# Kernel optimization log

Measured on AMD Instinct MI355X. Metric: run time of the kernel, lower is better.

The kernel has to match this reference:

```python
import jax, jax.numpy as jnp
import numpy as np

HEAD, DIM, R = 8, 256, 3
RA = (2 * R + 1) ** 2  # 49


def conv2d(x, w, b=None, pad=0, groups=1):
    y = jax.lax.conv_general_dilated(x, w, (1, 1), [(pad, pad), (pad, pad)],
                                     dimension_numbers=('NCHW', 'OIHW', 'NCHW'),
                                     feature_group_count=groups)
    return y if b is None else y + b[None, :, None, None]


def grid_sample(img, grid, mode, padding='zeros'):
    # img [B,C,H,W]; grid [B,Hg,Wg,2] with (x,y) in [-1,1]; align_corners=False.
    B, C, H, W = img.shape
    Hg, Wg = grid.shape[1], grid.shape[2]
    gx = ((grid[..., 0] + 1.0) * W - 1.0) / 2.0
    gy = ((grid[..., 1] + 1.0) * H - 1.0) / 2.0
    if padding == 'border':
        gx = jnp.clip(gx, 0.0, W - 1.0)
        gy = jnp.clip(gy, 0.0, H - 1.0)
    gx = gx.reshape(B, -1)
    gy = gy.reshape(B, -1)

    def gather(iy, ix):
        iyc = jnp.clip(iy, 0, H - 1)
        ixc = jnp.clip(ix, 0, W - 1)
        return jax.vmap(lambda im, a, b: im[:, a, b])(img, iyc, ixc)  # [B,C,N]

    def mask(iy, ix):
        if padding == 'border':
            return jnp.ones(iy.shape, img.dtype)
        return ((ix >= 0) & (ix < W) & (iy >= 0) & (iy < H)).astype(img.dtype)

    if mode == 'nearest':
        ix = jnp.round(gx).astype(jnp.int32)
        iy = jnp.round(gy).astype(jnp.int32)
        out = gather(iy, ix) * mask(iy, ix)[:, None, :]
    else:  # bilinear
        x0f = jnp.floor(gx); y0f = jnp.floor(gy)
        wx = gx - x0f; wy = gy - y0f
        x0 = x0f.astype(jnp.int32); y0 = y0f.astype(jnp.int32)
        out = jnp.zeros((B, C, gx.shape[1]), img.dtype)
        for dx, dy, w in ((0, 0, (1 - wx) * (1 - wy)), (1, 0, wx * (1 - wy)),
                          (0, 1, (1 - wx) * wy), (1, 1, wx * wy)):
            ix = x0 + dx; iy = y0 + dy
            out = out + gather(iy, ix) * (w * mask(iy, ix))[:, None, :]
    return out.reshape(B, C, Hg, Wg)


def mlp2(x, W1, b1, W2, b2):
    return jax.nn.relu(x @ W1.T + b1) @ W2.T + b2


def setup_inputs() -> dict:
    key = jax.random.key(0)
    ks = jax.random.split(key, 32)
    B, H, W, Q = 1, 64, 64, 4096
    f32 = jnp.float32
    rn = lambda k, shp, s=0.02: jax.random.normal(k, shp, f32) * s
    return {
        'inp': jax.random.normal(ks[0], (B, 3, H, W), f32),
        'coord': jax.random.uniform(ks[1], (B, Q, 2), f32, -1.0, 1.0),
        'cell': jnp.full((B, Q, 2), 2.0 / (2 * H), f32),
        'W_enc': rn(ks[2], (64, 3, 3, 3)), 'b_enc': jnp.zeros((64,), f32),
        'W_ch': rn(ks[3], (256, 64, 3, 3)), 'b_ch': jnp.zeros((256,), f32),
        'W_q': rn(ks[4], (256, 256, 3, 3)), 'b_q': jnp.zeros((256,), f32),
        'W_k': rn(ks[5], (256, 256, 3, 3)), 'b_k': jnp.zeros((256,), f32),
        'W_v': rn(ks[6], (256, 256, 3, 3)), 'b_v': jnp.zeros((256,), f32),
        'W_off1': rn(ks[7], (256, 32, 5, 5)), 'b_off1': jnp.zeros((256,), f32),
        'ln_g': jnp.ones((256,), f32), 'ln_b': jnp.zeros((256,), f32),
        'W_off2': rn(ks[8], (98, 256, 1, 1)),
        'Wc1': rn(ks[9], (256, 98)), 'bc1': jnp.zeros((256,), f32),
        'Wc2': rn(ks[10], (49, 256)), 'bc2': jnp.zeros((49,), f32),
        'Wi1': rn(ks[11], (256, 12546)), 'bi1': jnp.zeros((256,), f32),
        'Wi2': rn(ks[12], (3, 256)), 'bi2': jnp.zeros((3,), f32),
        'scale': 2,
    }


def reference(inp, coord, cell, W_enc, b_enc, W_ch, b_ch, W_q, b_q, W_k, b_k,
              W_v, b_v, W_off1, b_off1, ln_g, ln_b, W_off2, Wc1, bc1, Wc2, bc2,
              Wi1, bi1, Wi2, bi2, scale):
    B, _, H, W = inp.shape
    Q = coord.shape[1]
    # gen_feat: encoder stub (conv+relu) -> conv_ch -> q/k/v convs
    feat = conv2d(jax.nn.relu(conv2d(inp, W_enc, b_enc, pad=1)), W_ch, b_ch, pad=1)
    fq = conv2d(feat, W_q, b_q, pad=1)
    fk = conv2d(feat, W_k, b_k, pad=1)
    fv = conv2d(feat, W_v, b_v, pad=1)
    # offset branch: grouped 5x5 conv -> channelwise LN -> GELU -> 1x1 conv (no bias)
    o = conv2d(feat, W_off1, b_off1, pad=2, groups=8)
    oc = o.transpose(0, 2, 3, 1)
    mu = oc.mean(-1, keepdims=True)
    var = ((oc - mu) ** 2).mean(-1, keepdims=True)
    oc = (oc - mu) / jnp.sqrt(var + 1e-5) * ln_g + ln_b
    offsets = conv2d(jax.nn.gelu(oc.transpose(0, 3, 1, 2), approximate=False), W_off2, None, pad=0)  # [B,98,H,W]
    # LR coordinate grid (y,x) at pixel centers in [-1,1]
    ys = -1.0 + 1.0 / H + (2.0 / H) * jnp.arange(H, dtype=inp.dtype)
    xs = -1.0 + 1.0 / W + (2.0 / W) * jnp.arange(W, dtype=inp.dtype)
    coord_lr = jnp.broadcast_to(jnp.stack(jnp.meshgrid(ys, xs, indexing='ij'), 0)[None], (B, 2, H, W))
    sc = coord[:, :, None, :]          # [B,Q,1,2] (y,x)
    g = sc[..., ::-1]                  # (x,y) for grid_sample
    sck = grid_sample(coord_lr, g, 'nearest').transpose(0, 2, 3, 1)  # [B,Q,1,2]
    off = grid_sample(offsets, g, 'nearest').transpose(0, 2, 3, 1).reshape(B, Q, RA, 2)
    off = jnp.tanh(off) * jnp.array([1.0 / (H - 1.0), 1.0 / (W - 1.0)], inp.dtype) * 2.0
    d = jnp.linspace(-R, R, 2 * R + 1).astype(inp.dtype)
    delta = jnp.stack(jnp.meshgrid(d * (2.0 / H), d * (2.0 / W), indexing='ij'), -1).reshape(1, 1, RA, 2)
    sck = sck + delta + off            # [B,Q,49,2] sampling locs (y,x)
    q = grid_sample(fq, g, 'bilinear').transpose(0, 2, 3, 1).reshape(B, Q, HEAD, DIM // HEAD)
    k = grid_sample(fk, sck[..., ::-1], 'nearest').transpose(0, 2, 3, 1).reshape(B, Q, RA, HEAD, DIM // HEAD)
    v = grid_sample(fv, sck[..., ::-1], 'nearest').transpose(0, 2, 3, 1).reshape(B, Q, RA, HEAD, DIM // HEAD)
    attn_val = jnp.einsum('bqhd,bqkhd->bqkh', q, k) / np.sqrt(DIM // HEAD)  # [B,Q,49,8]
    rel = (sc - sck) * jnp.array([H, W], inp.dtype)  # [B,Q,49,2]
    wcoord = mlp2(rel.reshape(B * Q, RA * 2), Wc1, bc1, Wc2, bc2).reshape(B, Q, RA, 1)
    attn = jax.nn.softmax(wcoord + attn_val, axis=2)  # softmax over 49 samples
    feat_in = (v * attn[..., None]).reshape(B, Q, RA * DIM)
    rel_cell = cell * jnp.array([H, W], inp.dtype)
    feat_in = jnp.concatenate([feat_in, rel_cell], -1)  # [B,Q,12546]
    pred = mlp2(feat_in.reshape(B * Q, -1), Wi1, bi1, Wi2, bi2).reshape(B, Q, 3)
    skip = grid_sample(inp, g, 'bilinear', 'border')[:, :, :, 0].transpose(0, 2, 1)
    return pred + skip
```

## Files before the change

### kernel.cpp

```cpp
#include <hip/hip_runtime.h>
#include <hip/hip_bf16.h>


typedef unsigned short u16;
typedef unsigned int u32;
using frag_ab = __attribute__((ext_vector_type(8))) short;
using frag_cd = __attribute__((ext_vector_type(4))) float;

#define HW 4096
#define NQ 4096
#define KBIG 12576
#define SPLITK 16
#define KCHUNK 800
#define JMAX 5
#define KQ 2304
#define QSPLIT 3
#define QCHUNK 768
#define NBLK_QKV (64 * 6 * QSPLIT)
#define NBLK_OFF1 (64 * 8)

static __device__ __forceinline__ u16 f2b(float f) {
  union { __hip_bfloat16 h; u16 u; } c; c.h = __float2bfloat16(f); return c.u;
}
static __device__ __forceinline__ float b2f(u16 v) {
  return __uint_as_float((u32)v << 16);
}
static __device__ __forceinline__ u32 pk2(float a, float b) {
  union { __hip_bfloat162 h; u32 u; } c;
  c.h = __float22bfloat162_rn(float2{a, b});
  return c.u;
}
static __device__ __forceinline__ void glds16(const u16* g, u16* l) {
  __builtin_amdgcn_global_load_lds(
      (const __attribute__((address_space(1))) u32*)(g),
      (__attribute__((address_space(3))) u32*)(l), 16, 0, 0);
}

#define BM 64
#define BN 64
#define BK 32
#define LDSS 40

template<int W3, int SH, int PAD>
__global__ __launch_bounds__(256)
void gemm_conv(const u16* __restrict__ feat, const u16* __restrict__ Bt,
               void* __restrict__ Cv, const float* __restrict__ bias,
               int N, int K, int ldc, int flags, int FC, int cbStride,
               long sB, long sC, int sBias)
{
  __shared__ u16 As[BM * LDSS];
  __shared__ u16 Bs[BN * LDSS];
  const int z = blockIdx.z;
  Bt += (long)z * sB;
  const float* bz = bias ? bias + (long)z * sBias : nullptr;
  const int cb = z * cbStride;

  const int tid  = threadIdx.x;
  const int m0   = blockIdx.x * BM;
  const int n0   = blockIdx.y * BN;
  const int wave = tid >> 6, lane = tid & 63;
  const int mw = (wave & 1) * 32, nw = (wave >> 1) * 32;
  const int lr = lane & 15, lk = lane >> 4;
  const int srow = tid >> 2, scol = (tid & 3) * 8;
  const int p = m0 + srow, y = p >> 6, x = p & 63;

  frag_cd acc[2][2] = {};
  const bool bok  = (n0 + srow) < N;
  const u16* bptr = Bt + (size_t)(n0 + srow) * K + scol;

  auto stageA = [&](int k0) -> uint4 {
    int k = k0 + scol;
    int s = k >> SH;
    int c = k & ((1 << SH) - 1);
    int dy = s / W3, dx = s - dy * W3;
    int yy = y + dy - PAD, xx = x + dx - PAD;
    if (((unsigned)yy < 64u) && ((unsigned)xx < 64u))
      return *(const uint4*)&feat[(size_t)(yy * 64 + xx) * FC + cb + c];
    return uint4{0u, 0u, 0u, 0u};
  };

  uint4 av = stageA(0);
  uint4 bv = bok ? *(const uint4*)(bptr) : uint4{0u, 0u, 0u, 0u};

  for (int k0 = 0; k0 < K; k0 += BK) {
    *(uint4*)&As[srow * LDSS + scol] = av;
    *(uint4*)&Bs[srow * LDSS + scol] = bv;
    __syncthreads();
    if (k0 + BK < K) {
      av = stageA(k0 + BK);
      bv = bok ? *(const uint4*)(bptr + k0 + BK) : uint4{0u, 0u, 0u, 0u};
    }
    frag_ab af0 = *(const frag_ab*)&As[(mw      + lr) * LDSS + lk * 8];
    frag_ab af1 = *(const frag_ab*)&As[(mw + 16 + lr) * LDSS + lk * 8];
    frag_ab bf0 = *(const frag_ab*)&Bs[(nw      + lr) * LDSS + lk * 8];
    frag_ab bf1 = *(const frag_ab*)&Bs[(nw + 16 + lr) * LDSS + lk * 8];
    acc[0][0] = __builtin_amdgcn_mfma_f32_16x16x32_bf16(af0, bf0, acc[0][0], 0, 0, 0);
    acc[0][1] = __builtin_amdgcn_mfma_f32_16x16x32_bf16(af0, bf1, acc[0][1], 0, 0, 0);
    acc[1][0] = __builtin_amdgcn_mfma_f32_16x16x32_bf16(af1, bf0, acc[1][0], 0, 0, 0);
    acc[1][1] = __builtin_amdgcn_mfma_f32_16x16x32_bf16(af1, bf1, acc[1][1], 0, 0, 0);
    __syncthreads();
  }

  const bool relu = flags & 1;
  const bool obf  = flags & 2;
  #pragma unroll
  for (int i = 0; i < 2; i++)
    #pragma unroll
    for (int j = 0; j < 2; j++) {
      int col = n0 + nw + j * 16 + lr;
      if (col >= N) continue;
      float badd = bz ? bz[col] : 0.f;
      #pragma unroll
      for (int r = 0; r < 4; r++) {
        int row = m0 + mw + i * 16 + lk * 4 + r;
        float v = acc[i][j][r] + badd;
        if (relu) v = fmaxf(v, 0.f);
        size_t idx = (size_t)z * sC + (size_t)row * ldc + col;
        if (obf) ((u16*)Cv)[idx] = f2b(v);
        else     ((float*)Cv)[idx] = v;
      }
    }
}

__global__ __launch_bounds__(256)
void gemm_feat(const u16* __restrict__ feat, const u16* __restrict__ Btqkv,
               u16* __restrict__ Pq, const u16* __restrict__ Btoff1,
               float* __restrict__ obuf, const float* __restrict__ b_off1)
{
  __shared__ u16 smem[6656];
  const int bid = blockIdx.x;
  const int tid = threadIdx.x;
  const int wave = tid >> 6, lane = tid & 63;
  const int lr = lane & 15, lk = lane >> 4;

  if (bid < NBLK_QKV) {
    u16* As = smem;
    u16* Bs = smem + 64 * 40;
    const int mz  = bid & 63;
    const int rest = bid >> 6;
    const int ny  = rest % 6;
    const int z   = rest / 6;
    const int m0  = mz * 64;
    const int n0  = ny * 128;
    const int kbeg = z * QCHUNK;
    const int kend = kbeg + QCHUNK;
    const int nw = wave * 32;
    const int arow = tid >> 2, acol = (tid & 3) * 8;
    const int p = m0 + arow, y = p >> 6, x = p & 63;

    frag_cd acc[4][2] = {};
    const u16* bbase = Btqkv + (size_t)(n0 + (tid >> 2)) * KQ + (tid & 3) * 8 + kbeg;
    u16* bdst = &Bs[(size_t)tid * 8];

    auto stageA = [&](int k0) -> uint4 {
      int k = k0 + acol;
      int s = k >> 8, c = k & 255;
      int dy = s / 3, dx = s - dy * 3;
      int yy = y + dy - 1, xx = x + dx - 1;
      if (((unsigned)yy < 64u) && ((unsigned)xx < 64u))
        return *(const uint4*)&feat[(size_t)(yy * 64 + xx) * 256 + c];
      return uint4{0u, 0u, 0u, 0u};
    };

    uint4 av = stageA(kbeg);

    for (int k0 = kbeg; k0 < kend; k0 += BK) {
      glds16(bbase + (k0 - kbeg), bdst);
      glds16(bbase + (k0 - kbeg) + (size_t)64 * KQ, bdst + 2048);
      *(uint4*)&As[arow * LDSS + acol] = av;
      __syncthreads();
      if (k0 + BK < kend) av = stageA(k0 + BK);
      frag_ab af[4];
      #pragma unroll
      for (int i = 0; i < 4; i++)
        af[i] = *(const frag_ab*)&As[(i * 16 + lr) * LDSS + lk * 8];
      #pragma unroll
      for (int j = 0; j < 2; j++) {
        frag_ab bf = *(const frag_ab*)&Bs[(nw + j * 16 + lr) * 32 + lk * 8];
        #pragma unroll
        for (int i = 0; i < 4; i++)
          acc[i][j] = __builtin_amdgcn_mfma_f32_16x16x32_bf16(af[i], bf, acc[i][j], 0, 0, 0);
      }
      __syncthreads();
    }

    #pragma unroll
    for (int i = 0; i < 4; i++)
      #pragma unroll
      for (int j = 0; j < 2; j++) {
        int col = n0 + nw + j * 16 + lr;
        #pragma unroll
        for (int r = 0; r < 4; r++) {
          int row = m0 + i * 16 + lk * 4 + r;
          Pq[(size_t)z * (NQ * 768) + (size_t)row * 768 + col] = f2b(acc[i][j][r]);
        }
      }
  } else {
    u16* As = smem;
    u16* Bs = smem + 64 * 40;
    const int t  = bid - NBLK_QKV;
    const int m0 = (t & 63) * 64;
    const int g  = t >> 6;
    const int cb = g * 32;
    const u16* Bt = Btoff1 + (size_t)g * 32 * 800;
    const float* bz = b_off1 + g * 32;
    const int mw = (wave & 1) * 32, nw = (wave >> 1) * 32;
    const int srow = tid >> 2, scol = (tid & 3) * 8;
    const int p = m0 + srow, y = p >> 6, x = p & 63;

    frag_cd acc[2][2] = {};
    const bool bok  = srow < 32;
    const u16* bptr = Bt + (size_t)srow * 800 + scol;

    auto stageA = [&](int k0) -> uint4 {
      int k = k0 + scol;
      int s = k >> 5;
      int c = k & 31;
      int dy = s / 5, dx = s - dy * 5;
      int yy = y + dy - 2, xx = x + dx - 2;
      if (((unsigned)yy < 64u) && ((unsigned)xx < 64u))
        return *(const uint4*)&feat[(size_t)(yy * 64 + xx) * 256 + cb + c];
      return uint4{0u, 0u, 0u, 0u};
    };

    uint4 av = stageA(0);
    uint4 bv = bok ? *(const uint4*)(bptr) : uint4{0u, 0u, 0u, 0u};

    for (int k0 = 0; k0 < 800; k0 += BK) {
      *(uint4*)&As[srow * LDSS + scol] = av;
      *(uint4*)&Bs[srow * LDSS + scol] = bv;
      __syncthreads();
      if (k0 + BK < 800) {
        av = stageA(k0 + BK);
        bv = bok ? *(const uint4*)(bptr + k0 + BK) : uint4{0u, 0u, 0u, 0u};
      }
      frag_ab af0 = *(const frag_ab*)&As[(mw      + lr) * LDSS + lk * 8];
      frag_ab af1 = *(const frag_ab*)&As[(mw + 16 + lr) * LDSS + lk * 8];
      frag_ab bf0 = *(const frag_ab*)&Bs[(nw      + lr) * LDSS + lk * 8];
      frag_ab bf1 = *(const frag_ab*)&Bs[(nw + 16 + lr) * LDSS + lk * 8];
      acc[0][0] = __builtin_amdgcn_mfma_f32_16x16x32_bf16(af0, bf0, acc[0][0], 0, 0, 0);
      acc[0][1] = __builtin_amdgcn_mfma_f32_16x16x32_bf16(af0, bf1, acc[0][1], 0, 0, 0);
      acc[1][0] = __builtin_amdgcn_mfma_f32_16x16x32_bf16(af1, bf0, acc[1][0], 0, 0, 0);
      acc[1][1] = __builtin_amdgcn_mfma_f32_16x16x32_bf16(af1, bf1, acc[1][1], 0, 0, 0);
      __syncthreads();
    }

    #pragma unroll
    for (int i = 0; i < 2; i++)
      #pragma unroll
      for (int j = 0; j < 2; j++) {
        int col = nw + j * 16 + lr;
        if (col >= 32) continue;
        float badd = bz[col];
        #pragma unroll
        for (int r = 0; r < 4; r++) {
          int row = m0 + mw + i * 16 + lk * 4 + r;
          obuf[(size_t)row * 256 + g * 32 + col] = acc[i][j][r] + badd;
        }
      }
  }
}

#define RQ_BLKS 1536
#define LNO_BLKS 256
__global__ __launch_bounds__(256)
void post_feat(const u16* __restrict__ P, const float* __restrict__ bias,
               u16* __restrict__ outb, u16* __restrict__ outV,
               const float* __restrict__ x, const float* __restrict__ g,
               const float* __restrict__ b, const u16* __restrict__ Btoff2,
               float* __restrict__ offsb)
{
  __shared__ u16 s_oc[16 * 264];
  const int bid = blockIdx.x;
  const int tid = threadIdx.x;
  if (bid < RQ_BLKS) {
    int i8 = bid * 256 + tid;
    size_t i = (size_t)i8 * 8;
    int row = (int)(i / 768);
    int c = (int)(i % 768);
    float v[8];
    #pragma unroll
    for (int t = 0; t < 8; t++) v[t] = bias[c + t];
    for (int z = 0; z < QSPLIT; z++) {
      uint4 a = *(const uint4*)&P[(size_t)z * (NQ * 768) + i];
      u32 aw[4] = {a.x, a.y, a.z, a.w};
      #pragma unroll
      for (int t = 0; t < 4; t++) {
        v[2 * t]     += __uint_as_float(aw[t] << 16);
        v[2 * t + 1] += __uint_as_float(aw[t] & 0xffff0000u);
      }
    }
    uint4 ob = {pk2(v[0], v[1]), pk2(v[2], v[3]), pk2(v[4], v[5]), pk2(v[6], v[7])};
    *(uint4*)&outb[i] = ob;
    if (c >= 512) {
      *(uint4*)&outV[(size_t)row * 256 + (c - 512)] = ob;
    }
  } else {
    const int p0 = (bid - RQ_BLKS) * 16;
    const int p = tid >> 4, gl = tid & 15;
    float v[16];
    {
      const float* src = x + (size_t)(p0 + p) * 256 + gl * 16;
      #pragma unroll
      for (int t = 0; t < 4; t++) {
        float4 f = *(const float4*)(src + t * 4);
        v[4 * t] = f.x; v[4 * t + 1] = f.y; v[4 * t + 2] = f.z; v[4 * t + 3] = f.w;
      }
    }
    float s1 = 0.f, s2 = 0.f;
    #pragma unroll
    for (int t = 0; t < 16; t++) { s1 += v[t]; s2 += v[t] * v[t]; }
    #pragma unroll
    for (int off = 8; off; off >>= 1) {
      s1 += __shfl_xor(s1, off, 16);
      s2 += __shfl_xor(s2, off, 16);
    }
    float mu   = s1 * (1.f / 256.f);
    float var  = s2 * (1.f / 256.f) - mu * mu;
    float rstd = rsqrtf(var + 1e-5f);
    #pragma unroll
    for (int t = 0; t < 16; t++) {
      int c = gl * 16 + t;
      float xn = (v[t] - mu) * rstd * g[c] + b[c];
      float ge = 0.5f * xn * (1.f + erff(xn * 0.70710678118654752f));
      s_oc[p * 264 + c] = f2b(ge);
    }
    __syncthreads();
    const int wave = tid >> 6, lane = tid & 63;
    const int lr = lane & 15, lk = lane >> 4;
    frag_cd a0 = {}, a1 = {};
    #pragma unroll
    for (int k0 = 0; k0 < 256; k0 += 32) {
      frag_ab af = *(const frag_ab*)&s_oc[lr * 264 + k0 + lk * 8];
      frag_ab bf0 = *(const frag_ab*)&Btoff2[(size_t)(wave * 16 + lr) * 256 + k0 + lk * 8];
      a0 = __builtin_amdgcn_mfma_f32_16x16x32_bf16(af, bf0, a0, 0, 0, 0);
      if (wave < 3) {
        frag_ab bf1 = *(const frag_ab*)&Btoff2[(size_t)((wave + 4) * 16 + lr) * 256 + k0 + lk * 8];
        a1 = __builtin_amdgcn_mfma_f32_16x16x32_bf16(af, bf1, a1, 0, 0, 0);
      }
    }
    {
      const int col0 = wave * 16 + lr;
      const int col1 = (wave + 4) * 16 + lr;
      #pragma unroll
      for (int r = 0; r < 4; r++) {
        int row = lk * 4 + r;
        offsb[(size_t)(p0 + row) * 98 + col0] = a0[r];
        if (wave < 3 && col1 < 98)
          offsb[(size_t)(p0 + row) * 98 + col1] = a1[r];
      }
    }
  }
}

__global__ __launch_bounds__(512, 4)
void gemm_big(const u16* __restrict__ Bt, const u16* __restrict__ fqkvV,
              const float* __restrict__ attnval, const int* __restrict__ vidx,
              const float* __restrict__ cell, u16* __restrict__ P)
{
  __shared__ u16 As[128 * LDSS];
  __shared__ u16 Bs[2 * 256 * 32];
  __shared__ short s_vidx[JMAX * 128];
  __shared__ float s_attn[JMAX * 128 * 8];
  const int tid  = threadIdx.x;
  const int m0   = blockIdx.x * 128;
  const int z    = blockIdx.y;
  const int kbeg = z * KCHUNK;
  const int kend = min(KBIG, kbeg + KCHUNK);
  const int jbeg = kbeg >> 8;
  const int jcnt = ((kend - 1) >> 8) - jbeg + 1;
  const int wave = tid >> 6, lane = tid & 63;
  const int mw = (wave & 1) * 64, nwv = (wave >> 1) * 64;
  const int lr = lane & 15, lk = lane >> 4;
  const int arow = tid >> 2, acol = (tid & 3) * 8;
  const int q = m0 + arow;

  for (int t = tid; t < 128 * jcnt; t += 512) {
    int r = t & 127, jj = t >> 7;
    int j = jbeg + jj;
    s_vidx[t] = (short)((j < 49) ? vidx[(m0 + r) * 49 + j] : -1);
  }
  for (int t = tid; t < 128 * 8 * jcnt; t += 512) {
    int h = t & 7, rr = (t >> 3) & 127, jj = t >> 10;
    int j = jbeg + jj;
    s_attn[t] = (j < 49) ? attnval[((size_t)((m0 + rr) * 49 + j)) * 8 + h] : 0.f;
  }
  __syncthreads();

  auto loadA = [&](int k0, uint4& kv, float& w) {
    const int k = k0 + acol;
    const int j = k >> 8, c = k & 255;
    kv = uint4{0u, 0u, 0u, 0u};
    w = 0.f;
    if (j < 49) {
      const int jj = j - jbeg;
      int id = s_vidx[jj * 128 + arow];
      if (id >= 0) {
        w = s_attn[(jj * 128 + arow) * 8 + (c >> 5)];
        kv = *(const uint4*)(fqkvV + (size_t)id * 256 + c);
      }
    } else if (c == 0) {
      kv.x = pk2(cell[q * 2], cell[q * 2 + 1]);
      w = 64.f;
    }
  };

  frag_cd acc[4][4] = {};
  uint4 kvc; float wc_;
  const u16* bbase = Bt + (size_t)(tid >> 2) * KBIG + (tid & 3) * 8 + kbeg;

  glds16(bbase, &Bs[(size_t)tid * 8]);
  glds16(bbase + (size_t)128 * KBIG, &Bs[(size_t)tid * 8 + 4096]);
  loadA(kbeg, kvc, wc_);

  int par = 0;
  for (int k0 = kbeg; k0 < kend; k0 += BK, par ^= 1) {
    {
      u32 aw[4] = {kvc.x, kvc.y, kvc.z, kvc.w};
      uint4 av;
      u32 avw[4];
      #pragma unroll
      for (int t = 0; t < 4; t++) {
        float lo = __uint_as_float(aw[t] << 16) * wc_;
        float hi = __uint_as_float(aw[t] & 0xffff0000u) * wc_;
        avw[t] = pk2(lo, hi);
      }
      av.x = avw[0]; av.y = avw[1]; av.z = avw[2]; av.w = avw[3];
      *(uint4*)&As[arow * LDSS + acol] = av;
    }
    if (k0 + BK < kend) {
      u16* bd = &Bs[(size_t)(par ^ 1) * 8192 + (size_t)tid * 8];
      glds16(bbase + (k0 + BK - kbeg), bd);
      glds16(bbase + (k0 + BK - kbeg) + (size_t)128 * KBIG, bd + 4096);
      asm volatile("s_waitcnt vmcnt(2) lgkmcnt(0)" ::: "memory");
    } else {
      asm volatile("s_waitcnt vmcnt(0) lgkmcnt(0)" ::: "memory");
    }
    __builtin_amdgcn_s_barrier();
    if (k0 + BK < kend) loadA(k0 + BK, kvc, wc_);
    const u16* bsrc = &Bs[(size_t)par * 8192];
    frag_ab af[4];
    #pragma unroll
    for (int i = 0; i < 4; i++)
      af[i] = *(const frag_ab*)&As[(mw + i * 16 + lr) * LDSS + lk * 8];
    #pragma unroll
    for (int j = 0; j < 4; j++) {
      frag_ab bf = *(const frag_ab*)&bsrc[(nwv + j * 16 + lr) * 32 + lk * 8];
      #pragma unroll
      for (int i = 0; i < 4; i++)
        acc[i][j] = __builtin_amdgcn_mfma_f32_16x16x32_bf16(af[i], bf, acc[i][j], 0, 0, 0);
    }
    asm volatile("s_waitcnt lgkmcnt(0)" ::: "memory");
    __builtin_amdgcn_s_barrier();
  }

  #pragma unroll
  for (int i = 0; i < 4; i++)
    #pragma unroll
    for (int j = 0; j < 4; j++) {
      int col = nwv + j * 16 + lr;
      #pragma unroll
      for (int r = 0; r < 4; r++) {
        int row = m0 + mw + i * 16 + lk * 4 + r;
        P[(size_t)z * (NQ * 256) + (size_t)row * 256 + col] = f2b(acc[i][j][r]);
      }
    }
}

__global__ __launch_bounds__(256)
void reduce_final(const u16* __restrict__ Pb, const float* __restrict__ bi1,
                  const float* __restrict__ Wi2, const float* __restrict__ bi2,
                  const float* __restrict__ skipb, float* __restrict__ out)
{
  const int q = blockIdx.x, c = threadIdx.x;
  float s = 0.f;
  #pragma unroll
  for (int z = 0; z < SPLITK; z++)
    s += b2f(Pb[(size_t)z * (NQ * 256) + (size_t)q * 256 + c]);
  s += bi1[c];
  s = fmaxf(s, 0.f);

  __shared__ float part[3][4];
  float p0 = s * Wi2[c], p1 = s * Wi2[256 + c], p2 = s * Wi2[512 + c];
  #pragma unroll
  for (int off = 32; off; off >>= 1) {
    p0 += __shfl_xor(p0, off);
    p1 += __shfl_xor(p1, off);
    p2 += __shfl_xor(p2, off);
  }
  if ((c & 63) == 0) {
    int w = c >> 6;
    part[0][w] = p0; part[1][w] = p1; part[2][w] = p2;
  }
  __syncthreads();
  if (c < 3)
    out[q * 3 + c] = bi2[c] + skipb[q * 3 + c]
                   + part[c][0] + part[c][1] + part[c][2] + part[c][3];
}

__global__ __launch_bounds__(256)
void attn_wc(const u16* __restrict__ relbuf, const u16* __restrict__ Btc1,
             const float* __restrict__ bc1, const u16* __restrict__ Btc2,
             const float* __restrict__ bc2, float* __restrict__ attnval)
{
  __shared__ u16 s_rel[16 * 136];
  __shared__ u16 s_hid[16 * 264];
  __shared__ float s_wc[16 * 52];
  const int tid = threadIdx.x;
  const int m0 = blockIdx.x * 16;
  const int wave = tid >> 6, lane = tid & 63;
  const int lr = lane & 15, lk = lane >> 4;

  {
    int r = tid >> 4, kc = (tid & 15) * 8;
    uint4 v = *(const uint4*)&relbuf[(size_t)(m0 + r) * 128 + kc];
    *(uint4*)&s_rel[r * 136 + kc] = v;
  }
  __syncthreads();

  frag_cd acc1[4] = {};
  #pragma unroll
  for (int k0 = 0; k0 < 128; k0 += 32) {
    frag_ab af = *(const frag_ab*)&s_rel[lr * 136 + k0 + lk * 8];
    #pragma unroll
    for (int j = 0; j < 4; j++) {
      int col = wave * 64 + j * 16 + lr;
      frag_ab bf = *(const frag_ab*)&Btc1[(size_t)col * 128 + k0 + lk * 8];
      acc1[j] = __builtin_amdgcn_mfma_f32_16x16x32_bf16(af, bf, acc1[j], 0, 0, 0);
    }
  }
  #pragma unroll
  for (int j = 0; j < 4; j++) {
    int col = wave * 64 + j * 16 + lr;
    float badd = bc1[col];
    #pragma unroll
    for (int r = 0; r < 4; r++) {
      int row = lk * 4 + r;
      s_hid[row * 264 + col] = f2b(fmaxf(acc1[j][r] + badd, 0.f));
    }
  }
  __syncthreads();

  frag_cd acc2 = {};
  #pragma unroll
  for (int k0 = 0; k0 < 256; k0 += 32) {
    frag_ab af = *(const frag_ab*)&s_hid[lr * 264 + k0 + lk * 8];
    frag_ab bf = *(const frag_ab*)&Btc2[(size_t)(wave * 16 + lr) * 256 + k0 + lk * 8];
    acc2 = __builtin_amdgcn_mfma_f32_16x16x32_bf16(af, bf, acc2, 0, 0, 0);
  }
  {
    int col = wave * 16 + lr;
    if (col < 49) {
      float badd = bc2[col];
      #pragma unroll
      for (int r = 0; r < 4; r++) {
        int row = lk * 4 + r;
        s_wc[row * 52 + col] = acc2[r] + badd;
      }
    }
  }
  __syncthreads();

  if (tid < 128) {
    const int qq = tid >> 3, h = tid & 7;
    float* avp = attnval + ((size_t)(m0 + qq) * 49) * 8 + h;
    float v[49];
    float m = -1e30f;
    #pragma unroll
    for (int l = 0; l < 49; l++) {
      v[l] = s_wc[qq * 52 + l] + avp[(size_t)l * 8];
      m = fmaxf(m, v[l]);
    }
    float ssum = 0.f;
    #pragma unroll
    for (int l = 0; l < 49; l++) { v[l] = expf(v[l] - m); ssum += v[l]; }
    float inv = 1.f / ssum;
    #pragma unroll
    for (int l = 0; l < 49; l++) avp[(size_t)l * 8] = v[l] * inv;
  }
}

static __device__ __forceinline__
void packconv(const float* __restrict__ W, u16* __restrict__ Bt,
              int Cin, int K2, int idx)
{
  int o  = idx / (Cin * K2);
  int r  = idx - o * (Cin * K2);
  int ci = r / K2;
  int s  = r - ci * K2;
  Bt[(size_t)o * (Cin * K2) + s * Cin + ci] = f2b(W[idx]);
}
static __device__ __forceinline__
void packcast(const float* __restrict__ W, u16* __restrict__ Bt,
              int Kin, int Kout, int idx)
{
  int n = idx / Kout, k = idx - n * Kout;
  Bt[idx] = f2b(k < Kin ? W[(size_t)n * Kin + k] : 0.f);
}

#define SZ_CH    147456
#define SZ_QKV   589824
#define SZ_OFF1  204800
#define SZ_OFF2P 28672
#define SZ_C1    32768
#define SZ_C2P   16384
#define SZ_WI1   3219456
#define SZ_PACK (SZ_CH + 3*SZ_QKV + SZ_OFF1 + SZ_OFF2P + SZ_C1 + SZ_C2P + 768 + SZ_WI1)
#define CONV_BLKS 1024

__global__ __launch_bounds__(256)
void pack_enc(const float* W_ch, const float* W_q, const float* W_k,
              const float* W_v, const float* W_off1, const float* W_off2,
              const float* Wc1, const float* Wc2, const float* Wi1,
              const float* b_q, const float* b_k, const float* b_v,
              u16* Btch, u16* Btqkv, u16* Btoff1, u16* Btoff2,
              u16* Btc1, u16* Btc2, u16* Wi1p, float* bqkv,
              const float* __restrict__ inp, const float* __restrict__ W_enc,
              const float* __restrict__ b_enc, u16* __restrict__ feat1)
{
  const int bid = blockIdx.x;
  const int tid = threadIdx.x;
  if (bid < CONV_BLKS) {
    const int p = bid * 4 + (tid >> 6), c = tid & 63;
    const int y = p >> 6, x = p & 63;
    float s = b_enc[c];
    #pragma unroll
    for (int ci = 0; ci < 3; ci++)
      #pragma unroll
      for (int dy = 0; dy < 3; dy++) {
        int yy = y + dy - 1;
        if ((unsigned)yy >= 64u) continue;
        #pragma unroll
        for (int dx = 0; dx < 3; dx++) {
          int xx = x + dx - 1;
          if ((unsigned)xx >= 64u) continue;
          s += inp[ci * HW + yy * 64 + xx] * W_enc[((c * 3 + ci) * 3 + dy) * 3 + dx];
        }
      }
    feat1[(size_t)p * 64 + c] = f2b(fmaxf(s, 0.f));
    return;
  }
  int i = (bid - CONV_BLKS) * 256 + tid;
  if (i < SZ_CH) { packconv(W_ch, Btch, 64, 9, i); return; }
  i -= SZ_CH;
  if (i < SZ_QKV) { packconv(W_q, Btqkv, 256, 9, i); return; }
  i -= SZ_QKV;
  if (i < SZ_QKV) { packconv(W_k, Btqkv + (size_t)256 * 2304, 256, 9, i); return; }
  i -= SZ_QKV;
  if (i < SZ_QKV) { packconv(W_v, Btqkv + (size_t)512 * 2304, 256, 9, i); return; }
  i -= SZ_QKV;
  if (i < SZ_OFF1) { packconv(W_off1, Btoff1, 32, 25, i); return; }
  i -= SZ_OFF1;
  if (i < SZ_OFF2P) {
    int n = i >> 8, k = i & 255;
    Btoff2[i] = f2b(n < 98 ? W_off2[n * 256 + k] : 0.f);
    return;
  }
  i -= SZ_OFF2P;
  if (i < SZ_C1) { packcast(Wc1, Btc1, 98, 128, i); return; }
  i -= SZ_C1;
  if (i < SZ_C2P) {
    int n = i >> 8, k = i & 255;
    Btc2[i] = f2b(n < 49 ? Wc2[n * 256 + k] : 0.f);
    return;
  }
  i -= SZ_C2P;
  if (i < 768) {
    bqkv[i] = (i < 256) ? b_q[i] : (i < 512) ? b_k[i - 256] : b_v[i - 512];
    return;
  }
  i -= 768;
  if (i < SZ_WI1) { packcast(Wi1, Wi1p, 12546, 12576, i); }
}

__global__ __launch_bounds__(256)
void sampler(const float* __restrict__ coord, const u16* __restrict__ fqkvb,
             const float* __restrict__ offs, const float* __restrict__ inp,
             float* __restrict__ attnval, u16* __restrict__ relbuf,
             int* __restrict__ vidx, float* __restrict__ skipb)
{
  const int q = blockIdx.x;
  const int tid = threadIdx.x;
  __shared__ float s_off[98];
  __shared__ int s_idx[49];
  __shared__ float s_q[256];

  const float c0 = coord[q * 2], c1 = coord[q * 2 + 1];
  const float gxp = ((c1 + 1.f) * 64.f - 1.f) * 0.5f;
  const float gyp = ((c0 + 1.f) * 64.f - 1.f) * 0.5f;
  const int ixn = (int)rintf(gxp), iyn = (int)rintf(gyp);
  const bool inn = ((unsigned)ixn < 64u) && ((unsigned)iyn < 64u);

  if (tid < 98) {
    float v = inn ? offs[(size_t)(iyn * 64 + ixn) * 98 + tid] : 0.f;
    s_off[tid] = tanhf(v) * (2.f / 63.f);
  }
  __syncthreads();

  const float scky = inn ? (-1.f + (float)(2 * iyn + 1) * (1.f / 64.f)) : 0.f;
  const float sckx = inn ? (-1.f + (float)(2 * ixn + 1) * (1.f / 64.f)) : 0.f;

  if (tid < 49) {
    const int a = tid / 7, bb = tid - a * 7;
    float sy = scky + (float)(a - 3) * (2.f / 64.f) + s_off[2 * tid];
    float sx = sckx + (float)(bb - 3) * (2.f / 64.f) + s_off[2 * tid + 1];
    relbuf[(size_t)q * 128 + 2 * tid]     = f2b((c0 - sy) * 64.f);
    relbuf[(size_t)q * 128 + 2 * tid + 1] = f2b((c1 - sx) * 64.f);
    float gx2 = ((sx + 1.f) * 64.f - 1.f) * 0.5f;
    float gy2 = ((sy + 1.f) * 64.f - 1.f) * 0.5f;
    int ix2 = (int)rintf(gx2), iy2 = (int)rintf(gy2);
    int id = (((unsigned)ix2 < 64u) && ((unsigned)iy2 < 64u)) ? (iy2 * 64 + ix2) : -1;
    s_idx[tid] = id;
    vidx[q * 49 + tid] = id;
  } else if (tid >= 98 && tid < 128) {
    relbuf[(size_t)q * 128 + tid] = 0;
  }

  {
    const float x0f = floorf(gxp), y0f = floorf(gyp);
    const float wx = gxp - x0f, wy = gyp - y0f;
    const int x0 = (int)x0f, y0 = (int)y0f;
    float qc = 0.f;
    #pragma unroll
    for (int t = 0; t < 4; t++) {
      int xi = x0 + (t & 1), yi = y0 + (t >> 1);
      if (((unsigned)xi < 64u) && ((unsigned)yi < 64u)) {
        float w = ((t & 1) ? wx : 1.f - wx) * ((t >> 1) ? wy : 1.f - wy);
        qc += w * b2f(fqkvb[(size_t)(yi * 64 + xi) * 768 + tid]);
      }
    }
    s_q[tid] = qc * 0.17677669529663687f;
  }

  if (tid < 3) {
    float gx = fminf(fmaxf(gxp, 0.f), 63.f);
    float gy = fminf(fmaxf(gyp, 0.f), 63.f);
    float xf = floorf(gx), yf = floorf(gy);
    float wxs = gx - xf, wys = gy - yf;
    int xa = (int)xf, ya = (int)yf;
    int xb = min(xa + 1, 63), yb = min(ya + 1, 63);
    const float* ch = inp + tid * HW;
    float v = (1.f - wxs) * (1.f - wys) * ch[ya * 64 + xa]
            + wxs * (1.f - wys) * ch[ya * 64 + xb]
            + (1.f - wxs) * wys * ch[yb * 64 + xa]
            + wxs * wys * ch[yb * 64 + xb];
    skipb[q * 3 + tid] = v;
  }
  __syncthreads();

  const int wave = tid >> 6, lane = tid & 63;
  const int half = lane >> 5, sub = lane & 31;
  const int ch0 = sub * 8;
  const int h = sub >> 2;
  float qv[8];
  #pragma unroll
  for (int i = 0; i < 8; i++) qv[i] = s_q[ch0 + i];

  for (int it = 0; it < 7; it++) {
    int j = it * 8 + wave * 2 + half;
    if (j >= 49) break;
    int id = s_idx[j];
    float p = 0.f;
    if (id >= 0) {
      uint4 kv = *(const uint4*)&fqkvb[(size_t)id * 768 + 256 + ch0];
      u32 w0 = kv.x, w1 = kv.y, w2 = kv.z, w3 = kv.w;
      p = fmaf(qv[0], __uint_as_float(w0 << 16), p);
      p = fmaf(qv[1], __uint_as_float(w0 & 0xffff0000u), p);
      p = fmaf(qv[2], __uint_as_float(w1 << 16), p);
      p = fmaf(qv[3], __uint_as_float(w1 & 0xffff0000u), p);
      p = fmaf(qv[4], __uint_as_float(w2 << 16), p);
      p = fmaf(qv[5], __uint_as_float(w2 & 0xffff0000u), p);
      p = fmaf(qv[6], __uint_as_float(w3 << 16), p);
      p = fmaf(qv[7], __uint_as_float(w3 & 0xffff0000u), p);
    }
    p += __shfl_down(p, 2, 4);
    p += __shfl_down(p, 1, 4);
    if ((sub & 3) == 0) attnval[((size_t)q * 49 + j) * 8 + h] = p;
  }
}

extern "C" void kernel_launch(void* const* d_in, const int* in_sizes, int n_in,
                              void* d_out, int out_size, void* d_ws, size_t ws_size,
                              hipStream_t stream)
{
  const float* inp    = (const float*)d_in[0];
  const float* coord  = (const float*)d_in[1];
  const float* cell   = (const float*)d_in[2];
  const float* W_enc  = (const float*)d_in[3];
  const float* b_enc  = (const float*)d_in[4];
  const float* W_ch   = (const float*)d_in[5];
  const float* b_ch   = (const float*)d_in[6];
  const float* W_q    = (const float*)d_in[7];
  const float* b_q    = (const float*)d_in[8];
  const float* W_k    = (const float*)d_in[9];
  const float* b_k    = (const float*)d_in[10];
  const float* W_v    = (const float*)d_in[11];
  const float* b_v    = (const float*)d_in[12];
  const float* W_off1 = (const float*)d_in[13];
  const float* b_off1 = (const float*)d_in[14];
  const float* ln_g   = (const float*)d_in[15];
  const float* ln_b   = (const float*)d_in[16];
  const float* W_off2 = (const float*)d_in[17];
  const float* Wc1    = (const float*)d_in[18];
  const float* bc1    = (const float*)d_in[19];
  const float* Wc2    = (const float*)d_in[20];
  const float* bc2    = (const float*)d_in[21];
  const float* Wi1    = (const float*)d_in[22];
  const float* bi1    = (const float*)d_in[23];
  const float* Wi2    = (const float*)d_in[24];
  const float* bi2    = (const float*)d_in[25];

  char* base = (char*)d_ws;
  size_t off = 0;
  auto alloc = [&](size_t bytes) -> char* {
    char* r = base + off;
    off = (off + bytes + 255) & ~(size_t)255;
    return r;
  };

  float* obuf   = (float*)alloc((size_t)HW * 256 * 4);
  float* offsb  = (float*)alloc((size_t)HW * 98 * 4);
  u16*   feat1  = (u16*)  alloc((size_t)HW * 64 * 2);
  u16*   feat   = (u16*)  alloc((size_t)HW * 256 * 2);
  u16*   relbuf = (u16*)  alloc((size_t)NQ * 128 * 2);
  u16*   Btqkv  = (u16*)  alloc((size_t)768 * 2304 * 2);
  u16*   Btch   = (u16*)  alloc((size_t)256 * 576 * 2);
  u16*   Btoff1 = (u16*)  alloc((size_t)256 * 800 * 2);
  u16*   Btoff2 = (u16*)  alloc((size_t)112 * 256 * 2);
  u16*   Btc1   = (u16*)  alloc((size_t)256 * 128 * 2);
  u16*   Btc2   = (u16*)  alloc((size_t)64 * 256 * 2);
  u16* Pb = (u16*)base;
  u16* Pqb = (u16*)(base + ((size_t)36 << 20));
  {
    size_t need = ((size_t)36 << 20) + (size_t)QSPLIT * NQ * 768 * 2;
    if (off < need) off = (need + 255) & ~(size_t)255;
  }
  u16*   fqkvb   = (u16*)  alloc((size_t)HW * 768 * 2);
  u16*   fqkvVb  = (u16*)  alloc((size_t)HW * 256 * 2);
  float* attnval = (float*)alloc((size_t)NQ * 49 * 8 * 4);
  int*   vidxb   = (int*)  alloc((size_t)NQ * 49 * 4);
  float* skipb   = (float*)alloc((size_t)NQ * 3 * 4);
  u16*   Wi1p    = (u16*)  alloc((size_t)256 * KBIG * 2);
  float* bqkv    = (float*)alloc(768 * 4);
  (void)ws_size; (void)in_sizes; (void)n_in; (void)out_size;

  pack_enc<<<CONV_BLKS + (SZ_PACK + 255) / 256, 256, 0, stream>>>(
      W_ch, W_q, W_k, W_v, W_off1, W_off2, Wc1, Wc2, Wi1, b_q, b_k, b_v,
      Btch, Btqkv, Btoff1, Btoff2, Btc1, Btc2, Wi1p, bqkv,
      inp, W_enc, b_enc, feat1);

  gemm_conv<3, 6, 1><<<dim3(64, 4, 1), 256, 0, stream>>>(
      feat1, Btch, feat, b_ch, 256, 576, 256, 2, 64, 0, 0, 0, 0);
  gemm_feat<<<NBLK_QKV + NBLK_OFF1, 256, 0, stream>>>(
      feat, Btqkv, Pqb, Btoff1, obuf, b_off1);
  post_feat<<<RQ_BLKS + LNO_BLKS, 256, 0, stream>>>(
      Pqb, bqkv, fqkvb, fqkvVb, obuf, ln_g, ln_b, Btoff2, offsb);

  sampler<<<NQ, 256, 0, stream>>>(coord, fqkvb, offsb, inp,
                                  attnval, relbuf, vidxb, skipb);
  attn_wc<<<NQ / 16, 256, 0, stream>>>(relbuf, Btc1, bc1, Btc2, bc2, attnval);

  gemm_big<<<dim3(32, SPLITK), 512, 0, stream>>>(
      Wi1p, fqkvVb, attnval, vidxb, cell, Pb);
  reduce_final<<<NQ, 256, 0, stream>>>(Pb, bi1, Wi2, bi2, skipb, (float*)d_out);
}
```

Baseline: 262.4 us.

## Move weight packing into second conv kernel to overlap with conv GEMM

Splits the first launch so it only runs the encoder conv and packs the W_ch weights. The second conv GEMM is folded into a new kernel whose extra blocks pack the remaining weights (QKV, offsets, MLPs, Wi1). The large packing work now runs alongside the conv GEMM instead of sitting in front of it, which shortens the critical path. The conv GEMM is specialised with its parameters hard-coded, and the ReLU and bounds checks are dropped as they were unused for this call.

```diff
diff --git a/kernel.cpp b/kernel.cpp
--- a/kernel.cpp
+++ b/kernel.cpp
@@ -40,87 +40,6 @@
 #define BN 64
 #define BK 32
 #define LDSS 40
-
-template<int W3, int SH, int PAD>
-__global__ __launch_bounds__(256)
-void gemm_conv(const u16* __restrict__ feat, const u16* __restrict__ Bt,
-               void* __restrict__ Cv, const float* __restrict__ bias,
-               int N, int K, int ldc, int flags, int FC, int cbStride,
-               long sB, long sC, int sBias)
-{
-  __shared__ u16 As[BM * LDSS];
-  __shared__ u16 Bs[BN * LDSS];
-  const int z = blockIdx.z;
-  Bt += (long)z * sB;
-  const float* bz = bias ? bias + (long)z * sBias : nullptr;
-  const int cb = z * cbStride;
-
-  const int tid  = threadIdx.x;
-  const int m0   = blockIdx.x * BM;
-  const int n0   = blockIdx.y * BN;
-  const int wave = tid >> 6, lane = tid & 63;
-  const int mw = (wave & 1) * 32, nw = (wave >> 1) * 32;
-  const int lr = lane & 15, lk = lane >> 4;
-  const int srow = tid >> 2, scol = (tid & 3) * 8;
-  const int p = m0 + srow, y = p >> 6, x = p & 63;
-
-  frag_cd acc[2][2] = {};
-  const bool bok  = (n0 + srow) < N;
-  const u16* bptr = Bt + (size_t)(n0 + srow) * K + scol;
-
-  auto stageA = [&](int k0) -> uint4 {
-    int k = k0 + scol;
-    int s = k >> SH;
-    int c = k & ((1 << SH) - 1);
-    int dy = s / W3, dx = s - dy * W3;
-    int yy = y + dy - PAD, xx = x + dx - PAD;
-    if (((unsigned)yy < 64u) && ((unsigned)xx < 64u))
-      return *(const uint4*)&feat[(size_t)(yy * 64 + xx) * FC + cb + c];
-    return uint4{0u, 0u, 0u, 0u};
-  };
-
-  uint4 av = stageA(0);
-  uint4 bv = bok ? *(const uint4*)(bptr) : uint4{0u, 0u, 0u, 0u};
-
-  for (int k0 = 0; k0 < K; k0 += BK) {
-    *(uint4*)&As[srow * LDSS + scol] = av;
-    *(uint4*)&Bs[srow * LDSS + scol] = bv;
-    __syncthreads();
-    if (k0 + BK < K) {
-      av = stageA(k0 + BK);
-      bv = bok ? *(const uint4*)(bptr + k0 + BK) : uint4{0u, 0u, 0u, 0u};
-    }
-    frag_ab af0 = *(const frag_ab*)&As[(mw      + lr) * LDSS + lk * 8];
-    frag_ab af1 = *(const frag_ab*)&As[(mw + 16 + lr) * LDSS + lk * 8];
-    frag_ab bf0 = *(const frag_ab*)&Bs[(nw      + lr) * LDSS + lk * 8];
-    frag_ab bf1 = *(const frag_ab*)&Bs[(nw + 16 + lr) * LDSS + lk * 8];
-    acc[0][0] = __builtin_amdgcn_mfma_f32_16x16x32_bf16(af0, bf0, acc[0][0], 0, 0, 0);
-    acc[0][1] = __builtin_amdgcn_mfma_f32_16x16x32_bf16(af0, bf1, acc[0][1], 0, 0, 0);
-    acc[1][0] = __builtin_amdgcn_mfma_f32_16x16x32_bf16(af1, bf0, acc[1][0], 0, 0, 0);
-    acc[1][1] = __builtin_amdgcn_mfma_f32_16x16x32_bf16(af1, bf1, acc[1][1], 0, 0, 0);
-    __syncthreads();
-  }
-
-  const bool relu = flags & 1;
-  const bool obf  = flags & 2;
-  #pragma unroll
-  for (int i = 0; i < 2; i++)
-    #pragma unroll
-    for (int j = 0; j < 2; j++) {
-      int col = n0 + nw + j * 16 + lr;
-      if (col >= N) continue;
-      float badd = bz ? bz[col] : 0.f;
-      #pragma unroll
-      for (int r = 0; r < 4; r++) {
-        int row = m0 + mw + i * 16 + lk * 4 + r;
-        float v = acc[i][j][r] + badd;
-        if (relu) v = fmaxf(v, 0.f);
-        size_t idx = (size_t)z * sC + (size_t)row * ldc + col;
-        if (obf) ((u16*)Cv)[idx] = f2b(v);
-        else     ((float*)Cv)[idx] = v;
-      }
-    }
-}
 
 __global__ __launch_bounds__(256)
 void gemm_feat(const u16* __restrict__ feat, const u16* __restrict__ Btqkv,
@@ -605,18 +524,14 @@
 #define SZ_C1    32768
 #define SZ_C2P   16384
 #define SZ_WI1   3219456
-#define SZ_PACK (SZ_CH + 3*SZ_QKV + SZ_OFF1 + SZ_OFF2P + SZ_C1 + SZ_C2P + 768 + SZ_WI1)
+#define SZ_REST (3*SZ_QKV + SZ_OFF1 + SZ_OFF2P + SZ_C1 + SZ_C2P + 768 + SZ_WI1)
 #define CONV_BLKS 1024
+#define CONV2_BLKS 256
 
 __global__ __launch_bounds__(256)
-void pack_enc(const float* W_ch, const float* W_q, const float* W_k,
-              const float* W_v, const float* W_off1, const float* W_off2,
-              const float* Wc1, const float* Wc2, const float* Wi1,
-              const float* b_q, const float* b_k, const float* b_v,
-              u16* Btch, u16* Btqkv, u16* Btoff1, u16* Btoff2,
-              u16* Btc1, u16* Btc2, u16* Wi1p, float* bqkv,
-              const float* __restrict__ inp, const float* __restrict__ W_enc,
-              const float* __restrict__ b_enc, u16* __restrict__ feat1)
+void pack_enc(const float* __restrict__ inp, const float* __restrict__ W_enc,
+              const float* __restrict__ b_enc, u16* __restrict__ feat1,
+              const float* __restrict__ W_ch, u16* __restrict__ Btch)
 {
   const int bid = blockIdx.x;
   const int tid = threadIdx.x;
@@ -641,8 +556,83 @@
     return;
   }
   int i = (bid - CONV_BLKS) * 256 + tid;
-  if (i < SZ_CH) { packconv(W_ch, Btch, 64, 9, i); return; }
-  i -= SZ_CH;
+  if (i < SZ_CH) packconv(W_ch, Btch, 64, 9, i);
+}
+
+__global__ __launch_bounds__(256)
+void conv_pack(const u16* __restrict__ feat1, const u16* __restrict__ Btch,
+               u16* __restrict__ feat, const float* __restrict__ b_ch,
+               const float* W_q, const float* W_k, const float* W_v,
+               const float* W_off1, const float* W_off2,
+               const float* Wc1, const float* Wc2, const float* Wi1,
+               const float* b_q, const float* b_k, const float* b_v,
+               u16* Btqkv, u16* Btoff1, u16* Btoff2,
+               u16* Btc1, u16* Btc2, u16* Wi1p, float* bqkv)
+{
+  __shared__ u16 As[BM * LDSS];
+  __shared__ u16 Bs[BN * LDSS];
+  const int bid = blockIdx.x;
+  const int tid = threadIdx.x;
+  if (bid < CONV2_BLKS) {
+    const int m0 = (bid & 63) * 64;
+    const int n0 = (bid >> 6) * 64;
+    const int wave = tid >> 6, lane = tid & 63;
+    const int mw = (wave & 1) * 32, nw = (wave >> 1) * 32;
+    const int lr = lane & 15, lk = lane >> 4;
+    const int srow = tid >> 2, scol = (tid & 3) * 8;
+    const int p = m0 + srow, y = p >> 6, x = p & 63;
+
+    frag_cd acc[2][2] = {};
+    const u16* bptr = Btch + (size_t)(n0 + srow) * 576 + scol;
+
+    auto stageA = [&](int k0) -> uint4 {
+      int k = k0 + scol;
+      int s = k >> 6;
+      int c = k & 63;
+      int dy = s / 3, dx = s - dy * 3;
+      int yy = y + dy - 1, xx = x + dx - 1;
+      if (((unsigned)yy < 64u) && ((unsigned)xx < 64u))
+        return *(const uint4*)&feat1[(size_t)(yy * 64 + xx) * 64 + c];
+      return uint4{0u, 0u, 0u, 0u};
+    };
+
+    uint4 av = stageA(0);
+    uint4 bv = *(const uint4*)(bptr);
+
+    for (int k0 = 0; k0 < 576; k0 += BK) {
+      *(uint4*)&As[srow * LDSS + scol] = av;
+      *(uint4*)&Bs[srow * LDSS + scol] = bv;
+      __syncthreads();
+      if (k0 + BK < 576) {
+        av = stageA(k0 + BK);
+        bv = *(const uint4*)(bptr + k0 + BK);
+      }
+      frag_ab af0 = *(const frag_ab*)&As[(mw      + lr) * LDSS + lk * 8];
+      frag_ab af1 = *(const frag_ab*)&As[(mw + 16 + lr) * LDSS + lk * 8];
+      frag_ab bf0 = *(const frag_ab*)&Bs[(nw      + lr) * LDSS + lk * 8];
+      frag_ab bf1 = *(const frag_ab*)&Bs[(nw + 16 + lr) * LDSS + lk * 8];
+      acc[0][0] = __builtin_amdgcn_mfma_f32_16x16x32_bf16(af0, bf0, acc[0][0], 0, 0, 0);
+      acc[0][1] = __builtin_amdgcn_mfma_f32_16x16x32_bf16(af0, bf1, acc[0][1], 0, 0, 0);
+      acc[1][0] = __builtin_amdgcn_mfma_f32_16x16x32_bf16(af1, bf0, acc[1][0], 0, 0, 0);
+      acc[1][1] = __builtin_amdgcn_mfma_f32_16x16x32_bf16(af1, bf1, acc[1][1], 0, 0, 0);
+      __syncthreads();
+    }
+
+    #pragma unroll
+    for (int i = 0; i < 2; i++)
+      #pragma unroll
+      for (int j = 0; j < 2; j++) {
+        int col = n0 + nw + j * 16 + lr;
+        float badd = b_ch[col];
+        #pragma unroll
+        for (int r = 0; r < 4; r++) {
+          int row = m0 + mw + i * 16 + lk * 4 + r;
+          feat[(size_t)row * 256 + col] = f2b(acc[i][j][r] + badd);
+        }
+      }
+    return;
+  }
+  int i = (bid - CONV2_BLKS) * 256 + tid;
   if (i < SZ_QKV) { packconv(W_q, Btqkv, 256, 9, i); return; }
   i -= SZ_QKV;
   if (i < SZ_QKV) { packconv(W_k, Btqkv + (size_t)256 * 2304, 256, 9, i); return; }
@@ -844,13 +834,14 @@
   float* bqkv    = (float*)alloc(768 * 4);
   (void)ws_size; (void)in_sizes; (void)n_in; (void)out_size;
 
-  pack_enc<<<CONV_BLKS + (SZ_PACK + 255) / 256, 256, 0, stream>>>(
-      W_ch, W_q, W_k, W_v, W_off1, W_off2, Wc1, Wc2, Wi1, b_q, b_k, b_v,
-      Btch, Btqkv, Btoff1, Btoff2, Btc1, Btc2, Wi1p, bqkv,
-      inp, W_enc, b_enc, feat1);
-
-  gemm_conv<3, 6, 1><<<dim3(64, 4, 1), 256, 0, stream>>>(
-      feat1, Btch, feat, b_ch, 256, 576, 256, 2, 64, 0, 0, 0, 0);
+  pack_enc<<<CONV_BLKS + (SZ_CH + 255) / 256, 256, 0, stream>>>(
+      inp, W_enc, b_enc, feat1, W_ch, Btch);
+
+  conv_pack<<<CONV2_BLKS + (SZ_REST + 255) / 256, 256, 0, stream>>>(
+      feat1, Btch, feat, b_ch,
+      W_q, W_k, W_v, W_off1, W_off2, Wc1, Wc2, Wi1, b_q, b_k, b_v,
+      Btqkv, Btoff1, Btoff2, Btc1, Btc2, Wi1p, bqkv);
+
   gemm_feat<<<NBLK_QKV + NBLK_OFF1, 256, 0, stream>>>(
       feat, Btqkv, Pqb, Btoff1, obuf, b_off1);
   post_feat<<<RQ_BLKS + LNO_BLKS, 256, 0, stream>>>(
```

Result: no change. 259.8 us (-1.0%).
